# Kernel tuning notes

Measured on AMD Instinct MI355X. Metric: run time of the kernel, lower is better.

## Reference

```python
import jax, jax.numpy as jnp
import numpy as np


def setup_inputs() -> dict:
    key = jax.random.key(0)
    ks = jax.random.split(key, 9)
    B, S, D = 8, 2048, 1024
    scale = 1.0 / np.sqrt(D)
    return {
        "q": jax.random.normal(ks[0], (B, S, D), jnp.float32),
        "k": jax.random.normal(ks[1], (B, S, D), jnp.float32),
        "v": jax.random.normal(ks[2], (B, S, D), jnp.float32),
        "Wq": jax.random.normal(ks[3], (D, D), jnp.float32) * scale,
        "bq": jax.random.normal(ks[4], (D,), jnp.float32) * scale,
        "Wk": jax.random.normal(ks[5], (D, D), jnp.float32) * scale,
        "bk": jax.random.normal(ks[6], (D,), jnp.float32) * scale,
        "Wv": jax.random.normal(ks[7], (D, D), jnp.float32) * scale,
        "bv": jax.random.normal(ks[8], (D,), jnp.float32) * scale,
    }


def reference(q, k, v, Wq, bq, Wk, bk, Wv, bv):
    residual = q
    # torch nn.Linear: y = x @ W^T + b
    qp = jnp.einsum('bsd,ed->bse', q, Wq) + bq
    kp = jnp.einsum('bsd,ed->bse', k, Wk) + bk
    vp = jnp.einsum('bsd,ed->bse', v, Wv) + bv
    d_k = kp.shape[-1]
    scores = jnp.einsum('bqd,bkd->bqk', qp, kp) / d_k  # non-standard: divide by d, not sqrt(d)
    # non-standard softmax over dim=1 (the QUERY axis)
    attn_probs = jax.nn.softmax(scores, axis=1)
    attn = jnp.einsum('bqk,bkd->bqd', attn_probs, vp)
    # second softmax over dim=1 (sequence axis) to produce weights
    attn_w = jax.nn.softmax(attn, axis=1)
    attn = attn + residual
    return (attn, attn_w)
```

## Files before the change

### kernel.cpp

```cpp
#include <hip/hip_runtime.h>

typedef __attribute__((ext_vector_type(2))) long lx2;
typedef __attribute__((ext_vector_type(4))) float f32x4;

__device__ __forceinline__ ushort f2bf(float f) {
  union { float f; unsigned u; } x; x.f = f;
  unsigned r = x.u + 0x7FFFu + ((x.u >> 16) & 1u);
  return (ushort)(r >> 16);
}
__device__ __forceinline__ float bf2f(ushort u) {
  union { unsigned u; float f; } x; x.u = ((unsigned)u) << 16;
  return x.f;
}

#if defined(__has_builtin)
#if __has_builtin(__builtin_amdgcn_cvt_pk_fp8_f32) && __has_builtin(__builtin_amdgcn_cvt_f32_fp8)
#define HAVE_HW_FP8 1
#endif
#endif

#ifdef HAVE_HW_FP8
__device__ __forceinline__ uint pk4_fp8(float f0, float f1, float f2, float f3) {
  int r = __builtin_amdgcn_cvt_pk_fp8_f32(f0, f1, 0, false);
  r = __builtin_amdgcn_cvt_pk_fp8_f32(f2, f3, r, true);
  return (uint)r;
}
#define FP8DEC(dw, sel) __builtin_amdgcn_cvt_f32_fp8((int)(dw), (sel))
#else
__device__ __forceinline__ unsigned char f2e4m3(float f) {
  unsigned u = __float_as_uint(f);
  unsigned s = (u >> 24) & 0x80;
  float a = fabsf(f);
  if (a != a) return (unsigned char)(s | 0x7f);
  if (a >= 448.f) return (unsigned char)(s | 0x7e);
  int ei;
  (void)frexpf(a, &ei);
  int E = ei + 6;
  if (E < 1) {
    int ki = (int)rintf(a * 512.f);
    if (ki >= 8) return (unsigned char)(s | 0x08);
    return (unsigned char)(s | ki);
  }
  float q = a * exp2f((float)(10 - E));
  int ki = (int)rintf(q);
  if (ki >= 16) { E++; ki = 8; }
  if (E > 15 || (E == 15 && ki > 14)) return (unsigned char)(s | 0x7e);
  return (unsigned char)(s | (E << 3) | (ki - 8));
}
__device__ __forceinline__ uint pk4_fp8(float f0, float f1, float f2, float f3) {
  return (uint)f2e4m3(f0) | ((uint)f2e4m3(f1) << 8) |
         ((uint)f2e4m3(f2) << 16) | ((uint)f2e4m3(f3) << 24);
}
__device__ __forceinline__ float e4m3dec(unsigned char b) {
  int E = (b >> 3) & 15, M = b & 7;
  float v = E ? ldexpf((float)(8 + M), E - 10) : ldexpf((float)M, -9);
  return (b & 0x80) ? -v : v;
}
#define FP8DEC(dw, sel) e4m3dec((unsigned char)(((dw) >> (8 * (sel))) & 0xff))
#endif

__device__ __forceinline__ void gload_lds16(const void* g, void* l) {
  __builtin_amdgcn_global_load_lds(
      (const __attribute__((address_space(1))) void*)g,
      (__attribute__((address_space(3))) void*)l, 16, 0, 0);
}

__global__ __launch_bounds__(256) void cvt3_fp8(
    const float* __restrict__ s0, const float* __restrict__ s1,
    const float* __restrict__ s2, uint* __restrict__ d0,
    uint* __restrict__ d1, uint* __restrict__ d2, long n) {
  const float* s = blockIdx.y == 0 ? s0 : (blockIdx.y == 1 ? s1 : s2);
  uint* d = blockIdx.y == 0 ? d0 : (blockIdx.y == 1 ? d1 : d2);
  const int lane = threadIdx.x & 63;
  const int w = threadIdx.x >> 6;
  const long wave_base = ((long)blockIdx.x * 4 + w) * 1024;
  if (wave_base >= n) return;
  float4 f[4];
#pragma unroll
  for (int j = 0; j < 4; ++j)
    f[j] = *(const float4*)(s + wave_base + j * 256 + lane * 4);
#pragma unroll
  for (int j = 0; j < 4; ++j)
    d[(wave_base >> 2) + j * 64 + lane] = pk4_fp8(f[j].x, f[j].y, f[j].z, f[j].w);
}

template<int BIAS_MODE, int SCALED, int REDUCE, int EXPOUT, int OUT_FP8, int PF32>
__global__ __launch_bounds__(1024, 4) void gemmF(
    const void* __restrict__ Av, const void* __restrict__ Bv,
    void* __restrict__ Cv, const float* __restrict__ bias,
    float* __restrict__ red_max, float* __restrict__ red_sum,
    int N, int K, long sA, long sB, long sC, float scale, int gm, int gn)
{
  extern __shared__ unsigned char lds[];

  const int nwg = gridDim.x;
  const int wg = blockIdx.x;
  const int cpx = nwg >> 3;
  const int wid_ = (wg & 7) * cpx + (wg >> 3);
  const int tiles = gm * gn;
  const int bz = wid_ / tiles;
  const int t2 = wid_ - bz * tiles;
  const int band = t2 / (gm << 2);
  const int r2 = t2 - band * (gm << 2);
  const int tile_m = (r2 >> 2) * 256;
  const int tile_n = ((band << 2) + (r2 & 3)) * 256;

  const unsigned char* Ab8 = (PF32 == 1) ? nullptr : (const unsigned char*)Av + (size_t)bz * sA;
  const float*         AbF = (PF32 == 1) ? (const float*)Av + (size_t)bz * sA : nullptr;
  const unsigned char* Bb8 = (PF32 == 2) ? nullptr : (const unsigned char*)Bv + (size_t)bz * sB;
  const float*         BbF = (PF32 == 2) ? (const float*)Bv + (size_t)bz * sB : nullptr;

  const int t = threadIdx.x;
  const int lane = t & 63;
  const int w = t >> 6;
  const int wr = w >> 2;
  const int wc = w & 3;

  f32x4 acc[4][4] = {};
  float4 R[4];

#define STAGE_FA(c, k0)                                                                \
    gload_lds16(Ab8 + (size_t)(tile_m + w * 16 + (lane & 15)) * K + (k0) +             \
                    (lane >> 4) * 16,                                                  \
                lds + (c) * 32768 + w * 1024)
#define STAGE_FB(c, k0)                                                                \
    gload_lds16(Bb8 + (size_t)(tile_n + w * 16 + (lane & 15)) * K + (k0) +             \
                    (lane >> 4) * 16,                                                  \
                lds + (c) * 32768 + 16384 + w * 1024)
#define PLOAD(PbF, tile_p, k0)                                                         \
  do {                                                                                 \
    const float* pp = (PbF) + (size_t)((tile_p) + w * 16 + (lane & 15)) * K +          \
                      (k0) + (lane >> 4) * 16;                                         \
    R[0] = *(const float4*)(pp);      R[1] = *(const float4*)(pp + 4);                 \
    R[2] = *(const float4*)(pp + 8);  R[3] = *(const float4*)(pp + 12);                \
  } while (0)
#define PWRITE(c, roff)                                                                \
  do {                                                                                 \
    uint4 o;                                                                           \
    o.x = pk4_fp8(R[0].x, R[0].y, R[0].z, R[0].w);                                     \
    o.y = pk4_fp8(R[1].x, R[1].y, R[1].z, R[1].w);                                     \
    o.z = pk4_fp8(R[2].x, R[2].y, R[2].z, R[2].w);                                     \
    o.w = pk4_fp8(R[3].x, R[3].y, R[3].z, R[3].w);                                     \
    *(uint4*)(lds + (c) * 32768 + (roff) + w * 1024 + lane * 16) = o;                  \
  } while (0)

  if constexpr (PF32 == 1) { STAGE_FB(0, 0); PLOAD(AbF, tile_m, 0); }
  else if constexpr (PF32 == 2) { STAGE_FA(0, 0); PLOAD(BbF, tile_n, 0); }
  else { STAGE_FA(0, 0); STAGE_FB(0, 0); }

  const int KT = K >> 6;
  for (int tt = 0; tt < KT; ++tt) {
    const int c = tt & 1;
    asm volatile("s_waitcnt vmcnt(0)" ::: "memory");
    if constexpr (PF32 == 1) {
      PWRITE(c, 0);
      asm volatile("s_waitcnt lgkmcnt(0)" ::: "memory");
    } else if constexpr (PF32 == 2) {
      PWRITE(c, 16384);
      asm volatile("s_waitcnt lgkmcnt(0)" ::: "memory");
    }
    __builtin_amdgcn_s_barrier();
    if (tt + 1 < KT) {
      const int k0n = (tt + 1) << 6;
      if constexpr (PF32 == 1) { STAGE_FB(c ^ 1, k0n); PLOAD(AbF, tile_m, k0n); }
      else if constexpr (PF32 == 2) { STAGE_FA(c ^ 1, k0n); PLOAD(BbF, tile_n, k0n); }
      else { STAGE_FA(c ^ 1, k0n); STAGE_FB(c ^ 1, k0n); }
    }
    lx2 aA[4], bB[4];
#pragma unroll
    for (int mi = 0; mi < 4; ++mi)
      aA[mi] = *(const lx2*)(lds + c * 32768 + (wr * 4 + mi) * 1024 + lane * 16);
#pragma unroll
    for (int nf = 0; nf < 4; ++nf)
      bB[nf] = *(const lx2*)(lds + c * 32768 + 16384 + (wc * 4 + nf) * 1024 + lane * 16);
    asm volatile("s_waitcnt lgkmcnt(0)" ::: "memory");
    __builtin_amdgcn_sched_barrier(0);
    __builtin_amdgcn_s_setprio(1);
#pragma unroll
    for (int kk = 0; kk < 2; ++kk)
#pragma unroll
      for (int mi = 0; mi < 4; ++mi)
#pragma unroll
        for (int nf = 0; nf < 4; ++nf)
          acc[mi][nf] = __builtin_amdgcn_mfma_f32_16x16x32_fp8_fp8(
              aA[mi][kk], bB[nf][kk], acc[mi][nf], 0, 0, 0);
    __builtin_amdgcn_s_setprio(0);
  }
#undef STAGE_FA
#undef STAGE_FB
#undef PLOAD
#undef PWRITE

  float sm2[4] = {0.f, 0.f, 0.f, 0.f};
  const int g5 = ((lane >> 4) & 3) << 5;
  int ccl[4]; float bcn[4];
#pragma unroll
  for (int nf = 0; nf < 4; ++nf) {
    ccl[nf] = wc * 64 + nf * 16 + (lane & 15);
    bcn[nf] = (BIAS_MODE == 1) ? bias[tile_n + ccl[nf]] : 0.f;
  }
#pragma unroll
  for (int h = 0; h < 2; ++h) {
    __syncthreads();
    if ((wr >> 1) == h) {
#pragma unroll
      for (int mi = 0; mi < 4; ++mi) {
#pragma unroll
        for (int j = 0; j < 4; ++j) {
          const int row = (wr & 1) * 64 + mi * 16 + ((lane >> 4) << 2) + j;
          float bcr = (BIAS_MODE == 2) ? bias[tile_m + h * 128 + row] : 0.f;
#pragma unroll
          for (int nf = 0; nf < 4; ++nf) {
            float val = acc[mi][nf][j];
            if (SCALED) val *= scale;
            if (BIAS_MODE == 1) val += bcn[nf];
            else if (BIAS_MODE == 2) val += bcr;
            if (EXPOUT) val = __expf(val);
            if (REDUCE == 2) sm2[nf] += val;
            *(ushort*)(lds + row * 512 + ((ccl[nf] * 2) ^ g5)) = f2bf(val);
          }
        }
      }
    }
    __syncthreads();
#pragma unroll
    for (int p = 0; p < 4; ++p) {
      int off = p * 16384 + t * 16;
      int row = off >> 9;
      int b = off & 511;
      int bs = b ^ (((row >> 2) & 3) << 5);
      f32x4 d = *(const f32x4*)(lds + row * 512 + bs);
      const int gr = tile_m + h * 128 + row;
      if (OUT_FP8) {
        const uint* dw = (const uint*)&d;
        float f0 = bf2f((ushort)(dw[0] & 0xffff)), f1 = bf2f((ushort)(dw[0] >> 16));
        float f2 = bf2f((ushort)(dw[1] & 0xffff)), f3 = bf2f((ushort)(dw[1] >> 16));
        float f4 = bf2f((ushort)(dw[2] & 0xffff)), f5 = bf2f((ushort)(dw[2] >> 16));
        float f6 = bf2f((ushort)(dw[3] & 0xffff)), f7 = bf2f((ushort)(dw[3] >> 16));
        uint2 o;
        o.x = pk4_fp8(f0, f1, f2, f3);
        o.y = pk4_fp8(f4, f5, f6, f7);
        *(uint2*)((unsigned char*)Cv + (size_t)bz * sC + (size_t)gr * N + tile_n + (b >> 1)) = o;
      } else {
        *(f32x4*)((ushort*)Cv + (size_t)bz * sC + (size_t)gr * N + tile_n + (b >> 1)) = d;
      }
    }
  }

  if constexpr (REDUCE == 2) {
    __syncthreads();
    float* sb = (float*)lds;
#pragma unroll
    for (int nf = 0; nf < 4; ++nf) {
      float s1 = sm2[nf] + __shfl_xor(sm2[nf], 16);
      float Ss = s1 + __shfl_xor(s1, 32);
      if ((lane >> 4) == nf) sb[wr * 256 + ccl[nf]] = Ss;
    }
    __syncthreads();
    if (t < 256) {
      size_t rb = ((size_t)bz * gm + (tile_m >> 8)) * N + tile_n + t;
      red_sum[rb] = sb[t] + sb[256 + t] + sb[512 + t] + sb[768 + t];
    }
  }
  if constexpr (REDUCE == 1) {
    __syncthreads();
    float* mb = (float*)lds;
    float* sb = (float*)lds + 1024;
#pragma unroll
    for (int nf = 0; nf < 4; ++nf) {
      float mx = -1e30f;
#pragma unroll
      for (int mi = 0; mi < 4; ++mi)
#pragma unroll
        for (int j = 0; j < 4; ++j) {
          float val = acc[mi][nf][j];
          if (SCALED) val *= scale;
          mx = fmaxf(mx, val);
        }
      float m1 = fmaxf(mx, __shfl_xor(mx, 16));
      float M = fmaxf(m1, __shfl_xor(m1, 32));
      float sm = 0.f;
#pragma unroll
      for (int mi = 0; mi < 4; ++mi)
#pragma unroll
        for (int j = 0; j < 4; ++j) {
          float val = acc[mi][nf][j];
          if (SCALED) val *= scale;
          sm += __expf(val - M);
        }
      float s1 = sm + __shfl_xor(sm, 16);
      float Ss = s1 + __shfl_xor(s1, 32);
      if ((lane >> 4) == nf) {
        mb[wr * 256 + ccl[nf]] = M;
        sb[wr * 256 + ccl[nf]] = Ss;
      }
    }
    __syncthreads();
    if (t < 256) {
      float M = fmaxf(fmaxf(mb[t], mb[256 + t]), fmaxf(mb[512 + t], mb[768 + t]));
      float Ss = sb[t] * __expf(mb[t] - M) + sb[256 + t] * __expf(mb[256 + t] - M) +
                 sb[512 + t] * __expf(mb[512 + t] - M) + sb[768 + t] * __expf(mb[768 + t] - M);
      size_t rb = ((size_t)bz * gm + (tile_m >> 8)) * N + tile_n + t;
      red_max[rb] = M;
      red_sum[rb] = Ss;
    }
  }
}

__global__ __launch_bounds__(256) void combine_c(
    const float* __restrict__ red_sum, float* __restrict__ cvec, int cols, int nch)
{
  const int b = blockIdx.y;
  const int c = blockIdx.x * 256 + threadIdx.x;
  float Z = 0.f;
  for (int ch = 0; ch < nch; ++ch)
    Z += red_sum[((size_t)b * nch + ch) * cols + c];
  cvec[(size_t)b * cols + c] = 1024.f / Z;
}

__global__ __launch_bounds__(256) void scale_v(
    const uint2* __restrict__ vpT, const float* __restrict__ cvec,
    uint2* __restrict__ vs, int S, long DS)
{
  const size_t i8 = (size_t)blockIdx.x * 256 + threadIdx.x;
  const size_t k8 = i8 * 8;
  const int b = (int)(k8 / DS);
  const int kcol = (int)(k8 % S);
  uint2 u = vpT[i8];
  const float* cb = cvec + (size_t)b * S + kcol;
  float f0 = FP8DEC(u.x, 0) * cb[0], f1 = FP8DEC(u.x, 1) * cb[1];
  float f2 = FP8DEC(u.x, 2) * cb[2], f3 = FP8DEC(u.x, 3) * cb[3];
  float f4 = FP8DEC(u.y, 0) * cb[4], f5 = FP8DEC(u.y, 1) * cb[5];
  float f6 = FP8DEC(u.y, 2) * cb[6], f7 = FP8DEC(u.y, 3) * cb[7];
  uint2 o;
  o.x = pk4_fp8(f0, f1, f2, f3);
  o.y = pk4_fp8(f4, f5, f6, f7);
  vs[i8] = o;
}

__global__ __launch_bounds__(256) void colsm_combine(
    const float* __restrict__ red_max, const float* __restrict__ red_sum,
    float* __restrict__ Mv, float* __restrict__ Zinv, int cols, int nch)
{
  const int b = blockIdx.y;
  const int c = blockIdx.x * 256 + threadIdx.x;
  float M = -1e30f, Z = 0.f;
  for (int ch = 0; ch < nch; ++ch) {
    size_t o = ((size_t)b * nch + ch) * cols + c;
    float m = red_max[o], s = red_sum[o];
    float nm = fmaxf(M, m);
    Z = Z * __expf(M - nm) + s * __expf(m - nm);
    M = nm;
  }
  Mv[(size_t)b * cols + c] = M;
  Zinv[(size_t)b * cols + c] = 1.f / Z;
}

__global__ __launch_bounds__(256) void final_emit(
    const ushort* __restrict__ attnB, const float* __restrict__ q,
    float* __restrict__ out0, float* __restrict__ out1,
    const float* __restrict__ Mv, const float* __restrict__ Zinv,
    int rows, int cols, int rpc)
{
  const int b = blockIdx.y;
  const int ch = blockIdx.z;
  const size_t base = (size_t)b * rows * cols;
  const int c4 = (blockIdx.x * 256 + threadIdx.x) * 4;
  const int r0 = ch * rpc;
  float M[4], Zi[4];
#pragma unroll
  for (int i = 0; i < 4; ++i) {
    M[i] = Mv[(size_t)b * cols + c4 + i];
    Zi[i] = Zinv[(size_t)b * cols + c4 + i];
  }
  for (int r = r0; r < r0 + rpc; ++r) {
    size_t o = base + (size_t)r * cols + c4;
    ushort4 u = *(const ushort4*)(attnB + o);
    float4 qv = *(const float4*)(q + o);
    float a0 = bf2f(u.x), a1 = bf2f(u.y), a2 = bf2f(u.z), a3 = bf2f(u.w);
    float4 wv, s;
    wv.x = __expf(a0 - M[0]) * Zi[0];
    wv.y = __expf(a1 - M[1]) * Zi[1];
    wv.z = __expf(a2 - M[2]) * Zi[2];
    wv.w = __expf(a3 - M[3]) * Zi[3];
    s.x = a0 + qv.x; s.y = a1 + qv.y; s.z = a2 + qv.z; s.w = a3 + qv.w;
    *(float4*)(out1 + o) = wv;
    *(float4*)(out0 + o) = s;
  }
}

extern "C" void kernel_launch(void* const* d_in, const int* in_sizes, int n_in,
                              void* d_out, int out_size, void* d_ws, size_t ws_size,
                              hipStream_t stream) {
  const float* q  = (const float*)d_in[0];
  const float* k  = (const float*)d_in[1];
  const float* v  = (const float*)d_in[2];
  const float* Wq = (const float*)d_in[3];
  const float* bq = (const float*)d_in[4];
  const float* Wk = (const float*)d_in[5];
  const float* bk = (const float*)d_in[6];
  const float* Wv = (const float*)d_in[7];
  const float* bv = (const float*)d_in[8];
  float* out = (float*)d_out;

  const int B = 8, S = 2048, D = 1024;
  const long BS = (long)B * S;
  const long nQKV = BS * D;
  const long nW = (long)D * D;

  unsigned char* Wq8 = (unsigned char*)d_out;
  unsigned char* Wk8 = Wq8 + nW;
  unsigned char* Wv8 = Wk8 + nW;
  float* red_s_sum = (float*)((char*)d_out + (64ull << 20));
  float* c_s       = (float*)((char*)d_out + (66ull << 20));

  char* ws = (char*)d_ws;
  unsigned char* qp8   = (unsigned char*)ws;
  unsigned char* kp8   = (unsigned char*)(ws + (16ull << 20));
  unsigned char* vpT8  = (unsigned char*)(ws + (32ull << 20));
  unsigned char* vs8   = (unsigned char*)(ws + (48ull << 20));
  unsigned char* expS8 = (unsigned char*)(ws + (64ull << 20));
  ushort* attnB        = (ushort*)(ws + (96ull << 20));
  float* red_f_max = (float*)(ws + (128ull << 20));
  float* red_f_sum = (float*)(ws + (129ull << 20));
  float* Mf        = (float*)(ws + (130ull << 20));
  float* Zf        = (float*)(ws + (131ull << 20));

  const int SH = 65536;
  (void)hipFuncSetAttribute(reinterpret_cast<const void*>(&gemmF<1,0,0,0,1,1>),
                            hipFuncAttributeMaxDynamicSharedMemorySize, SH);
  (void)hipFuncSetAttribute(reinterpret_cast<const void*>(&gemmF<2,0,0,0,1,2>),
                            hipFuncAttributeMaxDynamicSharedMemorySize, SH);
  (void)hipFuncSetAttribute(reinterpret_cast<const void*>(&gemmF<0,1,2,1,1,0>),
                            hipFuncAttributeMaxDynamicSharedMemorySize, SH);
  (void)hipFuncSetAttribute(reinterpret_cast<const void*>(&gemmF<0,1,1,0,0,0>),
                            hipFuncAttributeMaxDynamicSharedMemorySize, SH);

  cvt3_fp8<<<dim3((unsigned)(nW / 4096), 3), 256, 0, stream>>>(
      Wq, Wk, Wv, (uint*)Wq8, (uint*)Wk8, (uint*)Wv8, nW);

  gemmF<1,0,0,0,1,1><<<dim3(64 * 4), 1024, SH, stream>>>(
      q, Wq8, qp8, bq, nullptr, nullptr, D, D, 0, 0, 0, 1.f, 64, 4);
  gemmF<1,0,0,0,1,1><<<dim3(64 * 4), 1024, SH, stream>>>(
      k, Wk8, kp8, bk, nullptr, nullptr, D, D, 0, 0, 0, 1.f, 64, 4);
  gemmF<2,0,0,0,1,2><<<dim3(4 * 8 * B), 1024, SH, stream>>>(
      Wv8, v, vpT8, bv, nullptr, nullptr, S, D, 0, (long)S * D, (long)D * S, 1.f, 4, 8);
  gemmF<0,1,2,1,1,0><<<dim3(8 * 8 * B), 1024, SH, stream>>>(
      qp8, kp8, expS8, nullptr, nullptr, red_s_sum,
      S, D, (long)S * D, (long)S * D, (long)S * S, 1.f / 1024.f, 8, 8);

  combine_c<<<dim3(S / 256, B), 256, 0, stream>>>(red_s_sum, c_s, S, 8);
  scale_v<<<dim3((int)(nQKV / (256 * 8))), 256, 0, stream>>>(
      (const uint2*)vpT8, c_s, (uint2*)vs8, S, (long)D * S);

  gemmF<0,1,1,0,0,0><<<dim3(8 * 4 * B), 1024, SH, stream>>>(
      expS8, vs8, attnB, nullptr, red_f_max, red_f_sum,
      D, S, (long)S * S, (long)D * S, (long)S * D, 1.f / 1024.f, 8, 4);

  colsm_combine<<<dim3(D / 256, B), 256, 0, stream>>>(red_f_max, red_f_sum, Mf, Zf, D, 8);
  final_emit<<<dim3(1, B, 128), 256, 0, stream>>>(attnB, q, out, out + nQKV, Mf, Zf, S, D, 16);

  (void)in_sizes; (void)n_in; (void)out_size; (void)ws_size;
}
```

Measured before the change: 349.4 us.

## Deepen fp32-operand prefetch pipeline and split A-fragment loads in fp8 GEMM

For the GEMM variants that convert one fp32 operand to fp8 in-kernel, the fp32 register prefetch now runs two K-tiles ahead. The convert-and-write to LDS happens after the barrier into the other buffer, so the global load latency no longer sits right before each barrier. The A fragments are also loaded from LDS in two halves around two MFMA batches, which lowers register pressure. The cost is more live registers for the extra in-flight prefetch and a more involved ordering between barriers and LDS buffers.

```diff
diff --git a/kernel.cpp b/kernel.cpp
--- a/kernel.cpp
+++ b/kernel.cpp
@@ -144,47 +144,100 @@
     *(uint4*)(lds + (c) * 32768 + (roff) + w * 1024 + lane * 16) = o;                  \
   } while (0)
 
-  if constexpr (PF32 == 1) { STAGE_FB(0, 0); PLOAD(AbF, tile_m, 0); }
-  else if constexpr (PF32 == 2) { STAGE_FA(0, 0); PLOAD(BbF, tile_n, 0); }
-  else { STAGE_FA(0, 0); STAGE_FB(0, 0); }
-
   const int KT = K >> 6;
+
+  if constexpr (PF32 == 0) {
+    STAGE_FA(0, 0); STAGE_FB(0, 0);
+  } else if constexpr (PF32 == 1) {
+    PLOAD(AbF, tile_m, 0);
+    STAGE_FB(0, 0);
+    asm volatile("s_waitcnt vmcnt(0)" ::: "memory");
+    PWRITE(0, 0);
+    asm volatile("s_waitcnt lgkmcnt(0)" ::: "memory");
+    if (KT > 1) PLOAD(AbF, tile_m, 64);
+  } else {
+    PLOAD(BbF, tile_n, 0);
+    STAGE_FA(0, 0);
+    asm volatile("s_waitcnt vmcnt(0)" ::: "memory");
+    PWRITE(0, 16384);
+    asm volatile("s_waitcnt lgkmcnt(0)" ::: "memory");
+    if (KT > 1) PLOAD(BbF, tile_n, 64);
+  }
+
   for (int tt = 0; tt < KT; ++tt) {
     const int c = tt & 1;
     asm volatile("s_waitcnt vmcnt(0)" ::: "memory");
-    if constexpr (PF32 == 1) {
-      PWRITE(c, 0);
-      asm volatile("s_waitcnt lgkmcnt(0)" ::: "memory");
-    } else if constexpr (PF32 == 2) {
-      PWRITE(c, 16384);
-      asm volatile("s_waitcnt lgkmcnt(0)" ::: "memory");
-    }
     __builtin_amdgcn_s_barrier();
     if (tt + 1 < KT) {
       const int k0n = (tt + 1) << 6;
-      if constexpr (PF32 == 1) { STAGE_FB(c ^ 1, k0n); PLOAD(AbF, tile_m, k0n); }
-      else if constexpr (PF32 == 2) { STAGE_FA(c ^ 1, k0n); PLOAD(BbF, tile_n, k0n); }
-      else { STAGE_FA(c ^ 1, k0n); STAGE_FB(c ^ 1, k0n); }
-    }
-    lx2 aA[4], bB[4];
-#pragma unroll
-    for (int mi = 0; mi < 4; ++mi)
-      aA[mi] = *(const lx2*)(lds + c * 32768 + (wr * 4 + mi) * 1024 + lane * 16);
-#pragma unroll
-    for (int nf = 0; nf < 4; ++nf)
-      bB[nf] = *(const lx2*)(lds + c * 32768 + 16384 + (wc * 4 + nf) * 1024 + lane * 16);
-    asm volatile("s_waitcnt lgkmcnt(0)" ::: "memory");
-    __builtin_amdgcn_sched_barrier(0);
-    __builtin_amdgcn_s_setprio(1);
-#pragma unroll
-    for (int kk = 0; kk < 2; ++kk)
+      if constexpr (PF32 == 1) {
+        PWRITE(c ^ 1, 0);
+        STAGE_FB(c ^ 1, k0n);
+        if (tt + 2 < KT) PLOAD(AbF, tile_m, (tt + 2) << 6);
+      } else if constexpr (PF32 == 2) {
+        PWRITE(c ^ 1, 16384);
+        STAGE_FA(c ^ 1, k0n);
+        if (tt + 2 < KT) PLOAD(BbF, tile_n, (tt + 2) << 6);
+      } else {
+        STAGE_FA(c ^ 1, k0n); STAGE_FB(c ^ 1, k0n);
+      }
+    }
+    if constexpr (PF32 == 0) {
+      lx2 aA[4], bB[4];
 #pragma unroll
       for (int mi = 0; mi < 4; ++mi)
-#pragma unroll
-        for (int nf = 0; nf < 4; ++nf)
-          acc[mi][nf] = __builtin_amdgcn_mfma_f32_16x16x32_fp8_fp8(
-              aA[mi][kk], bB[nf][kk], acc[mi][nf], 0, 0, 0);
-    __builtin_amdgcn_s_setprio(0);
+        aA[mi] = *(const lx2*)(lds + c * 32768 + (wr * 4 + mi) * 1024 + lane * 16);
+#pragma unroll
+      for (int nf = 0; nf < 4; ++nf)
+        bB[nf] = *(const lx2*)(lds + c * 32768 + 16384 + (wc * 4 + nf) * 1024 + lane * 16);
+      asm volatile("s_waitcnt lgkmcnt(0)" ::: "memory");
+      __builtin_amdgcn_sched_barrier(0);
+      __builtin_amdgcn_s_setprio(1);
+#pragma unroll
+      for (int kk = 0; kk < 2; ++kk)
+#pragma unroll
+        for (int mi = 0; mi < 4; ++mi)
+#pragma unroll
+          for (int nf = 0; nf < 4; ++nf)
+            acc[mi][nf] = __builtin_amdgcn_mfma_f32_16x16x32_fp8_fp8(
+                aA[mi][kk], bB[nf][kk], acc[mi][nf], 0, 0, 0);
+      __builtin_amdgcn_s_setprio(0);
+    } else {
+      lx2 aAh[2], bB[4];
+#pragma unroll
+      for (int nf = 0; nf < 4; ++nf)
+        bB[nf] = *(const lx2*)(lds + c * 32768 + 16384 + (wc * 4 + nf) * 1024 + lane * 16);
+#pragma unroll
+      for (int i = 0; i < 2; ++i)
+        aAh[i] = *(const lx2*)(lds + c * 32768 + (wr * 4 + i) * 1024 + lane * 16);
+      asm volatile("s_waitcnt lgkmcnt(0)" ::: "memory");
+      __builtin_amdgcn_sched_barrier(0);
+      __builtin_amdgcn_s_setprio(1);
+#pragma unroll
+      for (int kk = 0; kk < 2; ++kk)
+#pragma unroll
+        for (int mi = 0; mi < 2; ++mi)
+#pragma unroll
+          for (int nf = 0; nf < 4; ++nf)
+            acc[mi][nf] = __builtin_amdgcn_mfma_f32_16x16x32_fp8_fp8(
+                aAh[mi][kk], bB[nf][kk], acc[mi][nf], 0, 0, 0);
+      __builtin_amdgcn_s_setprio(0);
+#pragma unroll
+      for (int i = 0; i < 2; ++i)
+        aAh[i] = *(const lx2*)(lds + c * 32768 + (wr * 4 + 2 + i) * 1024 + lane * 16);
+      asm volatile("s_waitcnt lgkmcnt(0)" ::: "memory");
+      __builtin_amdgcn_sched_barrier(0);
+      __builtin_amdgcn_s_setprio(1);
+#pragma unroll
+      for (int kk = 0; kk < 2; ++kk)
+#pragma unroll
+        for (int mi = 0; mi < 2; ++mi)
+#pragma unroll
+          for (int nf = 0; nf < 4; ++nf)
+            acc[2 + mi][nf] = __builtin_amdgcn_mfma_f32_16x16x32_fp8_fp8(
+                aAh[mi][kk], bB[nf][kk], acc[2 + mi][nf], 0, 0, 0);
+      __builtin_amdgcn_s_setprio(0);
+    }
   }
 #undef STAGE_FA
 #undef STAGE_FB
```

Measured after the change: 342.0 us. -2.1%, faster.
